# Kernel optimization log

Hardware: AMD Instinct MI355X
Metric: run time of the kernel (lower is better)

Reference implementation:

```python
import jax, jax.numpy as jnp
import numpy as np

E = 500_000
H = 128
L = 3
N = 10_000


def setup_inputs() -> dict:
    key = jax.random.key(0)
    ks = jax.random.split(key, 9)
    s = 1.0 / np.sqrt(H)  # torch Linear default init scale
    return {
        "m": jax.random.normal(ks[0], (E, H), dtype=jnp.float32),
        "edge_index": jax.random.randint(ks[1], (2, E), 0, N, dtype=jnp.int64),
        "n_nodes": N,
        "W1": jax.random.uniform(ks[2], (L, H, H), jnp.float32, -s, s),
        "b1": jax.random.uniform(ks[3], (L, H), jnp.float32, -s, s),
        "W2": jax.random.uniform(ks[4], (L, H, H), jnp.float32, -s, s),
        "b2": jax.random.uniform(ks[5], (L, H), jnp.float32, -s, s),
        "Wlin": jax.random.uniform(ks[6], (H, H), jnp.float32, -s, s),
        "blin": jax.random.uniform(ks[7], (H,), jnp.float32, -s, s),
    }


def reference(m, edge_index, n_nodes, W1, b1, W2, b2, Wlin, blin):
    act = jax.nn.silu
    # Pre-activation residual stack: x + lin2(act(lin1(act(x))))
    for i in range(W1.shape[0]):
        h = act(m) @ W1[i].T + b1[i]
        m = m + (act(h) @ W2[i].T + b2[i])
    m = act(m @ Wlin.T + blin)  # [E, H]
    # scatter-add edge messages into target nodes (edge_index[1])
    out = jax.ops.segment_sum(m, edge_index[1], num_segments=n_nodes)  # [N, H]
    return out
```

## Files before the change

### kernel.cpp

```cpp
#include <hip/hip_runtime.h>
#include <hip/hip_bf16.h>

#define HDIM 128
#define NSTAGE 7
#define CHUNK_LOG 13
#define CHUNK (1 << CHUNK_LOG)

typedef __bf16 bf16x8 __attribute__((ext_vector_type(8)));
typedef __bf16 bf16x2 __attribute__((ext_vector_type(2)));
typedef float floatx16 __attribute__((ext_vector_type(16)));
typedef float floatx4 __attribute__((ext_vector_type(4)));
typedef int intx4 __attribute__((ext_vector_type(4)));

__device__ __forceinline__ float silu_f(float x) {
    return x * __builtin_amdgcn_rcpf(1.0f + __expf(-x));
}

__device__ __forceinline__ int pack2(float a, float b) {
    bf16x2 h;
    h[0] = (__bf16)a;
    h[1] = (__bf16)b;
    return __builtin_bit_cast(int, h);
}

__device__ __forceinline__ void unpack2f(int p, float& x0, float& x1) {
    bf16x2 h = __builtin_bit_cast(bf16x2, p);
    x0 = (float)h[0];
    x1 = (float)h[1];
}

__device__ __forceinline__ bf16x8 frag_from(int w0, int w1, int w2, int w3) {
    intx4 v; v[0] = w0; v[1] = w1; v[2] = w2; v[3] = w3;
    return __builtin_bit_cast(bf16x8, v);
}

__device__ __forceinline__ void gload_lds16(const void* g, void* l) {
    __builtin_amdgcn_global_load_lds(
        (const __attribute__((address_space(1))) unsigned int*)g,
        (__attribute__((address_space(3))) unsigned int*)l, 16, 0, 0);
}

__global__ void convert_weights(const float* __restrict__ W1,
                                const float* __restrict__ W2,
                                const float* __restrict__ Wlin,
                                __bf16* __restrict__ dst) {
    int idx = blockIdx.x * blockDim.x + threadIdx.x;
    if (idx >= NSTAGE * HDIM * HDIM) return;
    int s    = idx >> 14;
    int rem  = idx & 16383;
    int mrow = rem >> 7;
    int k    = rem & 127;
    const float* src;
    if (s == 6) src = Wlin;
    else {
        int l = s >> 1;
        src = ((s & 1) ? W2 : W1) + l * HDIM * HDIM;
    }
    float v = src[mrow * HDIM + k];
    int khalf = k >> 6;
    int c     = (k >> 3) & 7;
    int dsti  = (s << 14) + (khalf << 13) + (mrow << 6)
              + (((c ^ (mrow & 7)) << 3) | (k & 7));
    dst[dsti] = (__bf16)v;
}

__global__ __launch_bounds__(1024) void hist_rank_kernel(
    const int* __restrict__ tgt,
    unsigned short* __restrict__ rank,
    int* __restrict__ hb,
    int E, int N)
{
    __shared__ int lh[10240];
    for (int i = threadIdx.x; i < N; i += 1024) lh[i] = 0;
    __syncthreads();
    int ebase = blockIdx.x << CHUNK_LOG;
    int eend  = min(ebase + CHUNK, E);
    for (int e = ebase + (int)threadIdx.x; e < eend; e += 1024) {
        int node = tgt[e];
        int r = atomicAdd(&lh[node], 1);
        rank[e] = (unsigned short)r;
    }
    __syncthreads();
    int* row = hb + (size_t)blockIdx.x * N;
    for (int i = threadIdx.x; i < N; i += 1024) row[i] = lh[i];
}

__global__ void colsum_kernel(const int* __restrict__ hb, int* __restrict__ tot,
                              int nblk, int N) {
    int n = blockIdx.x * blockDim.x + threadIdx.x;
    if (n >= N) return;
    int s = 0;
    for (int b = 0; b < nblk; ++b) s += hb[(size_t)b * N + n];
    tot[n] = s;
}

__global__ __launch_bounds__(1024) void scan_kernel(const int* __restrict__ hist,
                                                    int* __restrict__ cursor, int N) {
    __shared__ int part[1024];
    int t = threadIdx.x;
    int per = (N + 1023) >> 10;
    int lo = t * per, hi = min(lo + per, N);
    int s = 0;
    for (int i = lo; i < hi; ++i) s += hist[i];
    part[t] = s;
    __syncthreads();
    for (int d = 1; d < 1024; d <<= 1) {
        int v = (t >= d) ? part[t - d] : 0;
        __syncthreads();
        part[t] += v;
        __syncthreads();
    }
    int off = (t == 0) ? 0 : part[t - 1];
    for (int i = lo; i < hi; ++i) { cursor[i] = off; off += hist[i]; }
}

__global__ void offsets_kernel(int* __restrict__ hb, const int* __restrict__ base,
                               int nblk, int N) {
    int n = blockIdx.x * blockDim.x + threadIdx.x;
    if (n >= N) return;
    int run = base[n];
    for (int b = 0; b < nblk; ++b) {
        size_t idx = (size_t)b * N + n;
        int c = hb[idx];
        hb[idx] = run;
        run += c;
    }
}

__global__ void emit_perm_kernel(const int* __restrict__ tgt,
                                 const unsigned short* __restrict__ rank,
                                 const int* __restrict__ hb,
                                 int* __restrict__ perm, int* __restrict__ snode,
                                 int E, int N) {
    int e = blockIdx.x * blockDim.x + threadIdx.x;
    if (e >= E) return;
    int node = tgt[e];
    int b = e >> CHUNK_LOG;
    int pos = hb[(size_t)b * N + node] + (int)rank[e];
    perm[pos] = e;
    snode[pos] = node;
}

__global__ __launch_bounds__(256, 3) void fused_mlp_scatter(
    const float* __restrict__ m,
    const int* __restrict__ perm,
    const int* __restrict__ snode,
    const __bf16* __restrict__ wmats,
    const float* __restrict__ b1,
    const float* __restrict__ b2,
    const float* __restrict__ blin,
    float* __restrict__ out,
    int E, int ntiles)
{
    __shared__ __align__(16) char smem[34816];
    float* ybuf = (float*)smem;

    const int tid  = threadIdx.x;
    const int w    = tid >> 6;
    const int lane = tid & 63;
    const int l31  = lane & 31;
    const int half = lane >> 5;

    const int tile    = blockIdx.x * 4 + w;
    const bool activeW = (tile < ntiles);
    const int pos = tile * 32 + l31;
    const bool evalid = activeW && (pos < E);

    int eidx = 0, mynode = 0;
    if (evalid) { eidx = perm[pos]; mynode = snode[pos]; }

    int Xp[4][4][2];
    floatx16 acc[4];
    int bw[8][4];

    #define BUILD_BW(KS, VA0,VA1,VA2,VA3, VB0,VB1,VB2,VB3) do {              \
        int A0_ = pack2((VA0), (VA1)); int A1_ = pack2((VA2), (VA3));        \
        int B0_ = pack2((VB0), (VB1)); int B1_ = pack2((VB2), (VB3));        \
        int N0_ = half ? A0_ : B0_;  int N1_ = half ? A1_ : B1_;             \
        int S0_ = __shfl_xor(N0_, 32, 64);                                   \
        int S1_ = __shfl_xor(N1_, 32, 64);                                   \
        bw[KS][0] = half ? S0_ : A0_;  bw[KS][1] = half ? S1_ : A1_;         \
        bw[KS][2] = half ? B0_ : S0_;  bw[KS][3] = half ? B1_ : S1_;         \
    } while (0)

    #define STAGE_HALF(HS, BUF) do {                                         \
        const char* g_ = (const char*)wmats + ((HS) << 14) + tid * 16;       \
        char* l_ = smem + ((BUF) << 14) + tid * 16;                          \
        _Pragma("unroll")                                                    \
        for (int i_ = 0; i_ < 4; ++i_)                                       \
            gload_lds16(g_ + i_ * 4096, l_ + i_ * 4096);                     \
    } while (0)

    STAGE_HALF(0, 0);

    if (activeW) {
        const float* mrow = m + (size_t)eidx * HDIM;
        #pragma unroll
        for (int mb = 0; mb < 4; ++mb) {
            floatx4 xv[4];
            #pragma unroll
            for (int q = 0; q < 4; ++q)
                xv[q] = *(const floatx4*)(mrow + mb * 32 + q * 8 + half * 4);
            #pragma unroll
            for (int q = 0; q < 4; ++q) {
                Xp[mb][q][0] = pack2(xv[q][0], xv[q][1]);
                Xp[mb][q][1] = pack2(xv[q][2], xv[q][3]);
            }
            BUILD_BW(2 * mb,
                silu_f(xv[0][0]), silu_f(xv[0][1]), silu_f(xv[0][2]), silu_f(xv[0][3]),
                silu_f(xv[1][0]), silu_f(xv[1][1]), silu_f(xv[1][2]), silu_f(xv[1][3]));
            BUILD_BW(2 * mb + 1,
                silu_f(xv[2][0]), silu_f(xv[2][1]), silu_f(xv[2][2]), silu_f(xv[2][3]),
                silu_f(xv[3][0]), silu_f(xv[3][1]), silu_f(xv[3][2]), silu_f(xv[3][3]));
        }
    }

    #pragma unroll
    for (int s = 0; s < NSTAGE; ++s) {
        __syncthreads();
        STAGE_HALF(2 * s + 1, 1);
        if (activeW) {
            const float* bias = (s == 6) ? blin
                              : ((s & 1) ? b2 + (s >> 1) * HDIM
                                         : b1 + (s >> 1) * HDIM);
            #pragma unroll
            for (int mb = 0; mb < 4; ++mb)
                #pragma unroll
                for (int q = 0; q < 4; ++q) {
                    floatx4 bv = *(const floatx4*)(bias + mb * 32 + q * 8 + half * 4);
                    #pragma unroll
                    for (int j = 0; j < 4; ++j) acc[mb][q * 4 + j] = bv[j];
                }
            const __bf16* wl = (const __bf16*)smem;
            #pragma unroll
            for (int lks = 0; lks < 4; ++lks) {
                bf16x8 bfrag = frag_from(bw[lks][0], bw[lks][1], bw[lks][2], bw[lks][3]);
                int krl = lks * 2 + half;
                #pragma unroll
                for (int mb = 0; mb < 4; ++mb) {
                    int mr = mb * 32 + l31;
                    bf16x8 afrag = *(const bf16x8*)(&wl[(mr << 6) + ((krl ^ (mr & 7)) << 3)]);
                    acc[mb] = __builtin_amdgcn_mfma_f32_32x32x16_bf16(afrag, bfrag, acc[mb], 0, 0, 0);
                }
            }
        }

        __syncthreads();
        if (s < NSTAGE - 1) STAGE_HALF(2 * s + 2, 0);
        if (!activeW) continue;
        {
            const __bf16* wl = (const __bf16*)(smem + 16384);
            #pragma unroll
            for (int lks = 0; lks < 4; ++lks) {
                bf16x8 bfrag = frag_from(bw[4 + lks][0], bw[4 + lks][1],
                                         bw[4 + lks][2], bw[4 + lks][3]);
                int krl = lks * 2 + half;
                #pragma unroll
                for (int mb = 0; mb < 4; ++mb) {
                    int mr = mb * 32 + l31;
                    bf16x8 afrag = *(const bf16x8*)(&wl[(mr << 6) + ((krl ^ (mr & 7)) << 3)]);
                    acc[mb] = __builtin_amdgcn_mfma_f32_32x32x16_bf16(afrag, bfrag, acc[mb], 0, 0, 0);
                }
            }
        }

        if (s == 6) {
            #pragma unroll
            for (int mb = 0; mb < 4; ++mb)
                #pragma unroll
                for (int r = 0; r < 16; ++r)
                    acc[mb][r] = silu_f(acc[mb][r]);
        } else if ((s & 1) == 0) {
            #pragma unroll
            for (int ks = 0; ks < 8; ++ks) {
                int mb = ks >> 1, qa = (ks & 1) * 2, qb = qa + 1;
                BUILD_BW(ks,
                    silu_f(acc[mb][qa * 4 + 0]), silu_f(acc[mb][qa * 4 + 1]),
                    silu_f(acc[mb][qa * 4 + 2]), silu_f(acc[mb][qa * 4 + 3]),
                    silu_f(acc[mb][qb * 4 + 0]), silu_f(acc[mb][qb * 4 + 1]),
                    silu_f(acc[mb][qb * 4 + 2]), silu_f(acc[mb][qb * 4 + 3]));
            }
        } else {
            #pragma unroll
            for (int ks = 0; ks < 8; ++ks) {
                int mb = ks >> 1, qa = (ks & 1) * 2, qb = qa + 1;
                float va[4], vb[4];
                {
                    float x0, x1, x2, x3;
                    unpack2f(Xp[mb][qa][0], x0, x1);
                    unpack2f(Xp[mb][qa][1], x2, x3);
                    x0 += acc[mb][qa * 4 + 0]; x1 += acc[mb][qa * 4 + 1];
                    x2 += acc[mb][qa * 4 + 2]; x3 += acc[mb][qa * 4 + 3];
                    Xp[mb][qa][0] = pack2(x0, x1);
                    Xp[mb][qa][1] = pack2(x2, x3);
                    va[0] = (s == 5) ? x0 : silu_f(x0);
                    va[1] = (s == 5) ? x1 : silu_f(x1);
                    va[2] = (s == 5) ? x2 : silu_f(x2);
                    va[3] = (s == 5) ? x3 : silu_f(x3);
                }
                {
                    float x0, x1, x2, x3;
                    unpack2f(Xp[mb][qb][0], x0, x1);
                    unpack2f(Xp[mb][qb][1], x2, x3);
                    x0 += acc[mb][qb * 4 + 0]; x1 += acc[mb][qb * 4 + 1];
                    x2 += acc[mb][qb * 4 + 2]; x3 += acc[mb][qb * 4 + 3];
                    Xp[mb][qb][0] = pack2(x0, x1);
                    Xp[mb][qb][1] = pack2(x2, x3);
                    vb[0] = (s == 5) ? x0 : silu_f(x0);
                    vb[1] = (s == 5) ? x1 : silu_f(x1);
                    vb[2] = (s == 5) ? x2 : silu_f(x2);
                    vb[3] = (s == 5) ? x3 : silu_f(x3);
                }
                BUILD_BW(ks, va[0], va[1], va[2], va[3],
                             vb[0], vb[1], vb[2], vb[3]);
            }
        }
    }

    __syncthreads();
    if (activeW) {
        const int ebase = tile * 32;
        const int cnt = min(32, E - ebase);
        float* yrow = ybuf + (w * 32 + l31) * 68;
        const float* yb = ybuf + w * 32 * 68;
        #pragma unroll
        for (int p = 0; p < 2; ++p) {
            #pragma unroll
            for (int mbh = 0; mbh < 2; ++mbh) {
                int mb = 2 * p + mbh;
                #pragma unroll
                for (int q = 0; q < 4; ++q) {
                    int f0 = mbh * 32 + q * 8 + half * 4;
                    floatx4 v;
                    for (int j = 0; j < 4; ++j) v[j] = acc[mb][q * 4 + j];
                    *(floatx4*)(yrow + f0) = v;
                }
            }
            int cur = __builtin_amdgcn_readlane(mynode, 0);
            float a0 = 0.f;
            for (int e = 0; e < cnt; ++e) {
                int node = __builtin_amdgcn_readlane(mynode, e);
                if (node != cur) {
                    unsafeAtomicAdd(out + (size_t)cur * HDIM + p * 64 + lane, a0);
                    cur = node; a0 = 0.f;
                }
                a0 += yb[e * 68 + lane];
            }
            unsafeAtomicAdd(out + (size_t)cur * HDIM + p * 64 + lane, a0);
        }
    }
    #undef BUILD_BW
    #undef STAGE_HALF
}

extern "C" void kernel_launch(void* const* d_in, const int* in_sizes, int n_in,
                              void* d_out, int out_size, void* d_ws, size_t ws_size,
                              hipStream_t stream) {
    const float* m      = (const float*)d_in[0];
    const int* edge_idx = (const int*)d_in[1];
    const float* W1     = (const float*)d_in[3];
    const float* b1     = (const float*)d_in[4];
    const float* W2     = (const float*)d_in[5];
    const float* b2     = (const float*)d_in[6];
    const float* Wlin   = (const float*)d_in[7];
    const float* blin   = (const float*)d_in[8];

    int E = in_sizes[0] / HDIM;
    int N = out_size / HDIM;
    const int* tgt = edge_idx + E;

    int nblk = (E + CHUNK - 1) >> CHUNK_LOG;

    char* ws = (char*)d_ws;
    size_t off = 0;
    auto align_up = [](size_t v) { return (v + 255) & ~(size_t)255; };

    __bf16* wbf = (__bf16*)(ws + off);
    off = align_up(off + (size_t)NSTAGE * HDIM * HDIM * sizeof(__bf16));
    unsigned short* rank = (unsigned short*)(ws + off);
    off = align_up(off + (size_t)E * sizeof(unsigned short));
    int* hb = (int*)(ws + off);
    off = align_up(off + (size_t)nblk * N * sizeof(int));
    int* tot = (int*)(ws + off);
    off = align_up(off + (size_t)N * sizeof(int));
    int* base = (int*)(ws + off);
    off = align_up(off + (size_t)N * sizeof(int));
    int* perm = (int*)(ws + off);
    off = align_up(off + (size_t)E * sizeof(int));
    int* snode = (int*)(ws + off);
    off = align_up(off + (size_t)E * sizeof(int));

    hipMemsetAsync(d_out, 0, (size_t)out_size * sizeof(float), stream);

    convert_weights<<<(NSTAGE * HDIM * HDIM + 255) / 256, 256, 0, stream>>>(W1, W2, Wlin, wbf);

    hist_rank_kernel<<<nblk, 1024, 0, stream>>>(tgt, rank, hb, E, N);
    colsum_kernel<<<(N + 255) / 256, 256, 0, stream>>>(hb, tot, nblk, N);
    scan_kernel<<<1, 1024, 0, stream>>>(tot, base, N);
    offsets_kernel<<<(N + 255) / 256, 256, 0, stream>>>(hb, base, nblk, N);
    emit_perm_kernel<<<(E + 255) / 256, 256, 0, stream>>>(tgt, rank, hb, perm, snode, E, N);

    int ntiles  = (E + 31) / 32;
    int nblocks = (ntiles + 3) / 4;
    fused_mlp_scatter<<<nblocks, 256, 0, stream>>>(m, perm, snode, wbf, b1, b2, blin,
                                                   (float*)d_out, E, ntiles);
}
```

Baseline: 571.1 us.

## Triple-buffer weight staging with vmcnt-based barriers and LDS-cached biases

Moves the weight staging from two LDS buffers to three 16KB buffers, issuing async global-to-LDS loads one half-stage further ahead. Full __syncthreads are replaced by explicit s_waitcnt vmcnt plus raw s_barrier, so outstanding prefetches need not drain at every barrier. All seven bias vectors are preloaded into LDS once instead of being read from global memory at each stage. LDS use rises from about 34KB to about 52KB per block, which may limit residency under the 3-blocks launch bound. The hand-counted vmcnt values are fragile if other global loads are in flight.

New measurement: 545.4 us. -4.5%, faster.

```diff
diff --git a/kernel.cpp b/kernel.cpp
--- a/kernel.cpp
+++ b/kernel.cpp
@@ -152,8 +152,9 @@
     float* __restrict__ out,
     int E, int ntiles)
 {
-    __shared__ __align__(16) char smem[34816];
-    float* ybuf = (float*)smem;
+    __shared__ __align__(16) char smem[52736];
+    float* ybuf     = (float*)smem;
+    float* bias_lds = (float*)(smem + 49152);
 
     const int tid  = threadIdx.x;
     const int w    = tid >> 6;
@@ -167,7 +168,6 @@
     const bool evalid = activeW && (pos < E);
 
     int eidx = 0, mynode = 0;
-    if (evalid) { eidx = perm[pos]; mynode = snode[pos]; }
 
     int Xp[4][4][2];
     floatx16 acc[4];
@@ -192,6 +192,16 @@
     } while (0)
 
     STAGE_HALF(0, 0);
+    STAGE_HALF(1, 1);
+
+    if (evalid) { eidx = perm[pos]; mynode = snode[pos]; }
+
+    for (int i = tid; i < NSTAGE * HDIM; i += 256) {
+        int s = i >> 7, f = i & 127;
+        float v = (s == 6) ? blin[f]
+                : ((s & 1) ? b2[(s >> 1) * HDIM + f] : b1[(s >> 1) * HDIM + f]);
+        bias_lds[i] = v;
+    }
 
     if (activeW) {
         const float* mrow = m + (size_t)eidx * HDIM;
@@ -215,23 +225,29 @@
         }
     }
 
+    __syncthreads();
+
     #pragma unroll
     for (int s = 0; s < NSTAGE; ++s) {
-        __syncthreads();
-        STAGE_HALF(2 * s + 1, 1);
+        if (s > 0) {
+            asm volatile("s_waitcnt vmcnt(4)" ::: "memory");
+            __builtin_amdgcn_sched_barrier(0);
+            __builtin_amdgcn_s_barrier();
+            __builtin_amdgcn_sched_barrier(0);
+        }
+        if (2 * s + 2 <= 13) STAGE_HALF(2 * s + 2, (2 * s + 2) % 3);
+
         if (activeW) {
-            const float* bias = (s == 6) ? blin
-                              : ((s & 1) ? b2 + (s >> 1) * HDIM
-                                         : b1 + (s >> 1) * HDIM);
+            const float* bl = bias_lds + s * HDIM;
             #pragma unroll
             for (int mb = 0; mb < 4; ++mb)
                 #pragma unroll
                 for (int q = 0; q < 4; ++q) {
-                    floatx4 bv = *(const floatx4*)(bias + mb * 32 + q * 8 + half * 4);
+                    floatx4 bv = *(const floatx4*)(bl + mb * 32 + q * 8 + half * 4);
                     #pragma unroll
                     for (int j = 0; j < 4; ++j) acc[mb][q * 4 + j] = bv[j];
                 }
-            const __bf16* wl = (const __bf16*)smem;
+            const __bf16* wl = (const __bf16*)(smem + ((2 * s) % 3) * 16384);
             #pragma unroll
             for (int lks = 0; lks < 4; ++lks) {
                 bf16x8 bfrag = frag_from(bw[lks][0], bw[lks][1], bw[lks][2], bw[lks][3]);
@@ -245,11 +261,15 @@
             }
         }
 
-        __syncthreads();
-        if (s < NSTAGE - 1) STAGE_HALF(2 * s + 2, 0);
-        if (!activeW) continue;
-        {
-            const __bf16* wl = (const __bf16*)(smem + 16384);
+        if (s == 6) asm volatile("s_waitcnt vmcnt(0)" ::: "memory");
+        else        asm volatile("s_waitcnt vmcnt(4)" ::: "memory");
+        __builtin_amdgcn_sched_barrier(0);
+        __builtin_amdgcn_s_barrier();
+        __builtin_amdgcn_sched_barrier(0);
+        if (2 * s + 3 <= 13) STAGE_HALF(2 * s + 3, (2 * s + 3) % 3);
+
+        if (activeW) {
+            const __bf16* wl = (const __bf16*)(smem + ((2 * s + 1) % 3) * 16384);
             #pragma unroll
             for (int lks = 0; lks < 4; ++lks) {
                 bf16x8 bfrag = frag_from(bw[4 + lks][0], bw[4 + lks][1],
@@ -262,57 +282,57 @@
                     acc[mb] = __builtin_amdgcn_mfma_f32_32x32x16_bf16(afrag, bfrag, acc[mb], 0, 0, 0);
                 }
             }
-        }
-
-        if (s == 6) {
-            #pragma unroll
-            for (int mb = 0; mb < 4; ++mb)
-                #pragma unroll
-                for (int r = 0; r < 16; ++r)
-                    acc[mb][r] = silu_f(acc[mb][r]);
-        } else if ((s & 1) == 0) {
-            #pragma unroll
-            for (int ks = 0; ks < 8; ++ks) {
-                int mb = ks >> 1, qa = (ks & 1) * 2, qb = qa + 1;
-                BUILD_BW(ks,
-                    silu_f(acc[mb][qa * 4 + 0]), silu_f(acc[mb][qa * 4 + 1]),
-                    silu_f(acc[mb][qa * 4 + 2]), silu_f(acc[mb][qa * 4 + 3]),
-                    silu_f(acc[mb][qb * 4 + 0]), silu_f(acc[mb][qb * 4 + 1]),
-                    silu_f(acc[mb][qb * 4 + 2]), silu_f(acc[mb][qb * 4 + 3]));
-            }
-        } else {
-            #pragma unroll
-            for (int ks = 0; ks < 8; ++ks) {
-                int mb = ks >> 1, qa = (ks & 1) * 2, qb = qa + 1;
-                float va[4], vb[4];
-                {
-                    float x0, x1, x2, x3;
-                    unpack2f(Xp[mb][qa][0], x0, x1);
-                    unpack2f(Xp[mb][qa][1], x2, x3);
-                    x0 += acc[mb][qa * 4 + 0]; x1 += acc[mb][qa * 4 + 1];
-                    x2 += acc[mb][qa * 4 + 2]; x3 += acc[mb][qa * 4 + 3];
-                    Xp[mb][qa][0] = pack2(x0, x1);
-                    Xp[mb][qa][1] = pack2(x2, x3);
-                    va[0] = (s == 5) ? x0 : silu_f(x0);
-                    va[1] = (s == 5) ? x1 : silu_f(x1);
-                    va[2] = (s == 5) ? x2 : silu_f(x2);
-                    va[3] = (s == 5) ? x3 : silu_f(x3);
-                }
-                {
-                    float x0, x1, x2, x3;
-                    unpack2f(Xp[mb][qb][0], x0, x1);
-                    unpack2f(Xp[mb][qb][1], x2, x3);
-                    x0 += acc[mb][qb * 4 + 0]; x1 += acc[mb][qb * 4 + 1];
-                    x2 += acc[mb][qb * 4 + 2]; x3 += acc[mb][qb * 4 + 3];
-                    Xp[mb][qb][0] = pack2(x0, x1);
-                    Xp[mb][qb][1] = pack2(x2, x3);
-                    vb[0] = (s == 5) ? x0 : silu_f(x0);
-                    vb[1] = (s == 5) ? x1 : silu_f(x1);
-                    vb[2] = (s == 5) ? x2 : silu_f(x2);
-                    vb[3] = (s == 5) ? x3 : silu_f(x3);
-                }
-                BUILD_BW(ks, va[0], va[1], va[2], va[3],
-                             vb[0], vb[1], vb[2], vb[3]);
+
+            if (s == 6) {
+                #pragma unroll
+                for (int mb = 0; mb < 4; ++mb)
+                    #pragma unroll
+                    for (int r = 0; r < 16; ++r)
+                        acc[mb][r] = silu_f(acc[mb][r]);
+            } else if ((s & 1) == 0) {
+                #pragma unroll
+                for (int ks = 0; ks < 8; ++ks) {
+                    int mb = ks >> 1, qa = (ks & 1) * 2, qb = qa + 1;
+                    BUILD_BW(ks,
+                        silu_f(acc[mb][qa * 4 + 0]), silu_f(acc[mb][qa * 4 + 1]),
+                        silu_f(acc[mb][qa * 4 + 2]), silu_f(acc[mb][qa * 4 + 3]),
+                        silu_f(acc[mb][qb * 4 + 0]), silu_f(acc[mb][qb * 4 + 1]),
+                        silu_f(acc[mb][qb * 4 + 2]), silu_f(acc[mb][qb * 4 + 3]));
+                }
+            } else {
+                #pragma unroll
+                for (int ks = 0; ks < 8; ++ks) {
+                    int mb = ks >> 1, qa = (ks & 1) * 2, qb = qa + 1;
+                    float va[4], vb[4];
+                    {
+                        float x0, x1, x2, x3;
+                        unpack2f(Xp[mb][qa][0], x0, x1);
+                        unpack2f(Xp[mb][qa][1], x2, x3);
+                        x0 += acc[mb][qa * 4 + 0]; x1 += acc[mb][qa * 4 + 1];
+                        x2 += acc[mb][qa * 4 + 2]; x3 += acc[mb][qa * 4 + 3];
+                        Xp[mb][qa][0] = pack2(x0, x1);
+                        Xp[mb][qa][1] = pack2(x2, x3);
+                        va[0] = (s == 5) ? x0 : silu_f(x0);
+                        va[1] = (s == 5) ? x1 : silu_f(x1);
+                        va[2] = (s == 5) ? x2 : silu_f(x2);
+                        va[3] = (s == 5) ? x3 : silu_f(x3);
+                    }
+                    {
+                        float x0, x1, x2, x3;
+                        unpack2f(Xp[mb][qb][0], x0, x1);
+                        unpack2f(Xp[mb][qb][1], x2, x3);
+                        x0 += acc[mb][qb * 4 + 0]; x1 += acc[mb][qb * 4 + 1];
+                        x2 += acc[mb][qb * 4 + 2]; x3 += acc[mb][qb * 4 + 3];
+                        Xp[mb][qb][0] = pack2(x0, x1);
+                        Xp[mb][qb][1] = pack2(x2, x3);
+                        vb[0] = (s == 5) ? x0 : silu_f(x0);
+                        vb[1] = (s == 5) ? x1 : silu_f(x1);
+                        vb[2] = (s == 5) ? x2 : silu_f(x2);
+                        vb[3] = (s == 5) ? x3 : silu_f(x3);
+                    }
+                    BUILD_BW(ks, va[0], va[1], va[2], va[3],
+                                 vb[0], vb[1], vb[2], vb[3]);
+                }
             }
         }
     }
```
